# Kernel tuning notes

Measured on AMD Instinct MI355X. Metric: run time of the kernel, lower is better.

## Reference

```python
import jax, jax.numpy as jnp
import numpy as np

B = 8192
D_IN = 1024
D_H = 1024


def _lin(x, w, b):
    # torch nn.Linear: y = x @ w.T + b, w: [out, in]
    return x @ w.T + b


def setup_inputs() -> dict:
    key = jax.random.key(0)
    ks = iter(jax.random.split(key, 64))
    s = 0.02

    def w(shape):
        return (jax.random.normal(next(ks), shape, dtype=jnp.float32) * s)

    inp = {
        "x": jax.random.normal(next(ks), (B, D_IN), dtype=jnp.float32),
        "h_prev": jax.random.normal(next(ks), (B, D_H), dtype=jnp.float32),
        "c_prev": jax.random.normal(next(ks), (B, D_H), dtype=jnp.float32),
    }
    for name in ["Wi", "Wf", "Wo", "Wc", "Ws"]:
        inp[name + "_w"] = w((D_H, D_IN))
        inp[name + "_b"] = w((D_H,))
    for name in ["Ui", "Uf", "Uo", "Uc", "Us"]:
        inp[name + "_w"] = w((D_H, D_H))
        inp[name + "_b"] = w((D_H,))
    # alpha_mlp: Linear(in+h -> h), ReLU, Linear(h -> 1), Sigmoid
    inp["a1_w"] = w((D_H, D_IN + D_H)); inp["a1_b"] = w((D_H,))
    inp["a2_w"] = w((1, D_H)); inp["a2_b"] = w((1,))
    inp["r1_w"] = w((D_H, D_H)); inp["r1_b"] = w((D_H,))
    inp["r2_w"] = w((D_H, D_H)); inp["r2_b"] = w((D_H,))
    inp["r3_w"] = w((D_H, D_H)); inp["r3_b"] = w((D_H,))
    return inp


def reference(x, h_prev, c_prev,
              Wi_w, Wi_b, Wf_w, Wf_b, Wo_w, Wo_b, Wc_w, Wc_b, Ws_w, Ws_b,
              Ui_w, Ui_b, Uf_w, Uf_b, Uo_w, Uo_b, Uc_w, Uc_b, Us_w, Us_b,
              a1_w, a1_b, a2_w, a2_b,
              r1_w, r1_b, r2_w, r2_b, r3_w, r3_b):
    i_t = jax.nn.sigmoid(_lin(x, Wi_w, Wi_b) + _lin(h_prev, Ui_w, Ui_b))
    f_t = jax.nn.sigmoid(_lin(x, Wf_w, Wf_b) + _lin(h_prev, Uf_w, Uf_b))
    o_t = jax.nn.sigmoid(_lin(x, Wo_w, Wo_b) + _lin(h_prev, Uo_w, Uo_b))
    c_hat_t = jnp.tanh(_lin(x, Wc_w, Wc_b) + _lin(h_prev, Uc_w, Uc_b))

    combined = jnp.concatenate([x, h_prev], axis=-1)  # [B, D_IN + D_H]
    alpha_t = jax.nn.sigmoid(_lin(jax.nn.relu(_lin(combined, a1_w, a1_b)), a2_w, a2_b))  # [B, 1]

    s_t = jax.nn.sigmoid(_lin(x, Ws_w, Ws_b) + _lin(h_prev, Us_w, Us_b))

    c_t = f_t * c_prev + i_t * c_hat_t * s_t * alpha_t

    residual = _lin(jax.nn.relu(_lin(jax.nn.relu(_lin(h_prev, r1_w, r1_b)), r2_w, r2_b)), r3_w, r3_b)
    c_t = c_t + residual
    h_t = o_t * jnp.tanh(c_t)
    return (h_t, c_t)
```

## Files before the change

### kernel.cpp

```cpp
#include <hip/hip_runtime.h>
#include <hip/hip_bf16.h>

typedef __bf16 bf16;
typedef __bf16 bf16x8 __attribute__((ext_vector_type(8)));
typedef __bf16 bf16x4 __attribute__((ext_vector_type(4)));
typedef float f32x4 __attribute__((ext_vector_type(4)));

#define NBIG 7168
#define KBIG 2048

__device__ __forceinline__ float sigmoid_f(float x) { return 1.0f / (1.0f + __expf(-x)); }
__device__ __forceinline__ float tanh_f(float x) { return 1.0f - 2.0f / (__expf(2.0f * x) + 1.0f); }

__device__ __forceinline__ void gload_lds16(const bf16* g, bf16* lds) {
  __builtin_amdgcn_global_load_lds(
      (const __attribute__((address_space(1))) unsigned int*)g,
      (__attribute__((address_space(3))) unsigned int*)lds,
      16, 0, 0);
}


__global__ __launch_bounds__(256) void build_A(const float* __restrict__ x,
                                               const float* __restrict__ h,
                                               bf16* __restrict__ A) {
  const int i4 = blockIdx.x * 256 + threadIdx.x;
  const int o = i4 * 4;
  const int m = o >> 11;
  const int c = o & 2047;
  const float4 v = (c < 1024) ? *(const float4*)&x[(size_t)m * 1024 + c]
                              : *(const float4*)&h[(size_t)m * 1024 + (c - 1024)];
  bf16x4 b;
  b[0] = (bf16)v.x; b[1] = (bf16)v.y; b[2] = (bf16)v.z; b[3] = (bf16)v.w;
  *(bf16x4*)&A[(size_t)o] = b;
}

__global__ __launch_bounds__(256) void build_WG(
    const float* __restrict__ Wi, const float* __restrict__ Wf, const float* __restrict__ Wo,
    const float* __restrict__ Wc, const float* __restrict__ Ws,
    const float* __restrict__ Ui, const float* __restrict__ Uf, const float* __restrict__ Uo,
    const float* __restrict__ Uc, const float* __restrict__ Us,
    const float* __restrict__ a1w, const float* __restrict__ r1w, bf16* __restrict__ WG) {
  const int i4 = blockIdx.x * 256 + threadIdx.x;
  const int o = i4 * 4;
  const int n = o >> 11;
  const int c = o & 2047;
  const int g = n >> 10;
  const int r = n & 1023;
  float4 v;
  if (g < 5) {
    const float* Wp = g == 0 ? Wi : g == 1 ? Wf : g == 2 ? Wo : g == 3 ? Wc : Ws;
    const float* Up = g == 0 ? Ui : g == 1 ? Uf : g == 2 ? Uo : g == 3 ? Uc : Us;
    v = (c < 1024) ? *(const float4*)&Wp[(size_t)r * 1024 + c]
                   : *(const float4*)&Up[(size_t)r * 1024 + (c - 1024)];
  } else if (g == 5) {
    v = *(const float4*)&a1w[(size_t)r * 2048 + c];
  } else {
    if (c < 1024) { v.x = 0.f; v.y = 0.f; v.z = 0.f; v.w = 0.f; }
    else v = *(const float4*)&r1w[(size_t)r * 1024 + (c - 1024)];
  }
  bf16x4 b;
  b[0] = (bf16)v.x; b[1] = (bf16)v.y; b[2] = (bf16)v.z; b[3] = (bf16)v.w;
  *(bf16x4*)&WG[(size_t)o] = b;
}

__global__ __launch_bounds__(256) void build_bias(
    const float* __restrict__ Wib, const float* __restrict__ Wfb, const float* __restrict__ Wob,
    const float* __restrict__ Wcb, const float* __restrict__ Wsb,
    const float* __restrict__ Uib, const float* __restrict__ Ufb, const float* __restrict__ Uob,
    const float* __restrict__ Ucb, const float* __restrict__ Usb,
    const float* __restrict__ a1b, const float* __restrict__ r1b, float* __restrict__ bias) {
  const int n = blockIdx.x * 256 + threadIdx.x;
  if (n >= NBIG) return;
  const int g = n >> 10, r = n & 1023;
  float v;
  if (g < 5) {
    const float* Wb = g == 0 ? Wib : g == 1 ? Wfb : g == 2 ? Wob : g == 3 ? Wcb : Wsb;
    const float* Ub = g == 0 ? Uib : g == 1 ? Ufb : g == 2 ? Uob : g == 3 ? Ucb : Usb;
    v = Wb[r] + Ub[r];
  } else if (g == 5) v = a1b[r];
  else v = r1b[r];
  bias[n] = v;
}

__global__ __launch_bounds__(256) void f2b(const float* __restrict__ s, bf16* __restrict__ d,
                                           int n4) {
  const int i = blockIdx.x * 256 + threadIdx.x;
  if (i >= n4) return;
  const float4 v = *(const float4*)&s[(size_t)i * 4];
  bf16x4 b;
  b[0] = (bf16)v.x; b[1] = (bf16)v.y; b[2] = (bf16)v.z; b[3] = (bf16)v.w;
  *(bf16x4*)&d[(size_t)i * 4] = b;
}


#define BAR __builtin_amdgcn_s_barrier()
#define VM4 asm volatile("s_waitcnt vmcnt(4)" ::: "memory")
#define VM0 asm volatile("s_waitcnt vmcnt(0)" ::: "memory")
#define PRIO1 __builtin_amdgcn_s_setprio(1)
#define PRIO0 __builtin_amdgcn_s_setprio(0)

__global__ __launch_bounds__(256, 3) void gemm128(
    const bf16* __restrict__ A, int lda,
    const bf16* __restrict__ W, int ldw, int K,
    const float* __restrict__ bias,
    bf16* __restrict__ C, int ldc, int act_mode, int mtiles) {
  __shared__ __align__(16) bf16 sA[3][128 * 32];
  __shared__ __align__(16) bf16 sB[3][128 * 32];

  const int tid = threadIdx.x;
  const int lane = tid & 63;
  const int wv = tid >> 6;
  const int wr = wv >> 1, wc = wv & 1;

  int bmi, bni;
  if (gridDim.x == 3584) {
    const int xcd = blockIdx.x & 7;
    const int idx = blockIdx.x >> 3;
    bmi = (xcd >> 1) * 16 + idx / 28;
    bni = (xcd & 1) * 28 + idx % 28;
  } else {
    bmi = blockIdx.x % mtiles;
    bni = blockIdx.x / mtiles;
  }
  const int bm = bmi * 128;
  const int bn = bni * 128;

  const int srow = tid >> 2;
  const int scol = ((tid & 3) ^ ((tid >> 3) & 3)) * 8;
  const bf16* pA = A + (size_t)(bm + srow) * lda + scol;
  const bf16* pB = W + (size_t)(bn + srow) * ldw + scol;

  const int fr = lane & 15;
  const int lg = lane >> 4;
  const int sw16 = (lg ^ ((fr >> 1) & 3)) << 4;

  const int NT = K >> 5;

  f32x4 acc[4][4] = {};
  bf16x8 ar[4], br[4];

#define STGT(bb, tt)                                                \
  do {                                                              \
    const bf16* gA = pA + (size_t)(tt) * 32;                        \
    bf16* lA = &sA[bb][(wv * 16) * 32];                             \
    gload_lds16(gA, lA);                                            \
    gload_lds16(gA + (size_t)64 * lda, lA + 64 * 32);               \
    const bf16* gB = pB + (size_t)(tt) * 32;                        \
    bf16* lB = &sB[bb][(wv * 16) * 32];                             \
    gload_lds16(gB, lB);                                            \
    gload_lds16(gB + (size_t)64 * ldw, lB + 64 * 32);               \
  } while (0)
#define LDF(bb)                                                                  \
  do {                                                                           \
    _Pragma("unroll") for (int mi = 0; mi < 4; ++mi)                             \
        ar[mi] = *(const bf16x8*)((const char*)&sA[bb][0] +                      \
            (wr * 64 + mi * 16 + fr) * 64 + sw16);                               \
    _Pragma("unroll") for (int nj = 0; nj < 4; ++nj)                             \
        br[nj] = *(const bf16x8*)((const char*)&sB[bb][0] +                      \
            (wc * 64 + nj * 16 + fr) * 64 + sw16);                               \
  } while (0)
#define MM()                                                                     \
  do {                                                                           \
    _Pragma("unroll") for (int mi = 0; mi < 4; ++mi)                             \
    _Pragma("unroll") for (int nj = 0; nj < 4; ++nj)                             \
      acc[mi][nj] = __builtin_amdgcn_mfma_f32_16x16x32_bf16(                     \
          ar[mi], br[nj], acc[mi][nj], 0, 0, 0);                                 \
  } while (0)

  STGT(0, 0);
  STGT(1, 1);
  VM4; BAR;

  int bld = 0;
  int bst = 2;
  for (int t = 0; t + 2 < NT; ++t) {
    STGT(bst, t + 2);
    LDF(bld);
    PRIO1; MM(); PRIO0;
    VM4;
    BAR;
    bld = bld == 2 ? 0 : bld + 1;
    bst = bst == 2 ? 0 : bst + 1;
  }

  LDF(bld);
  PRIO1; MM(); PRIO0;
  VM0; BAR;
  bld = bld == 2 ? 0 : bld + 1;
  LDF(bld);
  PRIO1; MM(); PRIO0;

  const int rbase = lg * 4;
#pragma unroll
  for (int j = 0; j < 4; ++j) {
    const int n = bn + wc * 64 + j * 16 + fr;
    const float bv = bias[n];
    const int g = (act_mode == 0) ? (n >> 10) : (act_mode == 1 ? 100 : 101);
#pragma unroll
    for (int mi = 0; mi < 4; ++mi) {
      const size_t mrow = (size_t)(bm + wr * 64 + mi * 16 + rbase);
#pragma unroll
      for (int r = 0; r < 4; ++r) {
        float v = acc[mi][j][r] + bv;
        if (g == 3) v = tanh_f(v);
        else if (g < 5) v = sigmoid_f(v);
        else if (g < 7 || g == 100) v = fmaxf(v, 0.0f);
        C[(mrow + r) * (size_t)ldc + n] = (bf16)v;
      }
    }
  }
#undef STGT
#undef LDF
#undef MM
}

__global__ __launch_bounds__(256) void alpha_k(const bf16* __restrict__ G,
                                               const float* __restrict__ a2w,
                                               const float* __restrict__ a2b,
                                               float* __restrict__ alpha) {
  const int m = blockIdx.x * 4 + (threadIdx.x >> 6);
  const int lane = threadIdx.x & 63;
  const bf16* row = G + (size_t)m * NBIG + 5120 + lane * 16;
  const bf16x8 v0 = *(const bf16x8*)row;
  const bf16x8 v1 = *(const bf16x8*)(row + 8);
  const float* w = a2w + lane * 16;
  float s = 0.f;
#pragma unroll
  for (int e = 0; e < 8; ++e) s += (float)v0[e] * w[e] + (float)v1[e] * w[8 + e];
#pragma unroll
  for (int off = 32; off > 0; off >>= 1) s += __shfl_down(s, off, 64);
  if (lane == 0) alpha[m] = sigmoid_f(s + a2b[0]);
}

__global__ __launch_bounds__(256) void final_k(const bf16* __restrict__ G,
                                               const bf16* __restrict__ R3,
                                               const float* __restrict__ c_prev,
                                               const float* __restrict__ alpha,
                                               float* __restrict__ out) {
  const int idx = blockIdx.x * 256 + threadIdx.x;
  const int o = idx * 8;
  const int m = o >> 10;
  const int c = o & 1023;
  const size_t gb = (size_t)m * NBIG;
  const bf16x8 iv = *(const bf16x8*)&G[gb + c];
  const bf16x8 fv = *(const bf16x8*)&G[gb + 1024 + c];
  const bf16x8 ov = *(const bf16x8*)&G[gb + 2048 + c];
  const bf16x8 cv = *(const bf16x8*)&G[gb + 3072 + c];
  const bf16x8 sv = *(const bf16x8*)&G[gb + 4096 + c];
  const bf16x8 rv = *(const bf16x8*)&R3[(size_t)m * 1024 + c];
  const float al = alpha[m];
  const float* cp = &c_prev[(size_t)m * 1024 + c];
  float hbuf[8], cbuf[8];
#pragma unroll
  for (int e = 0; e < 8; ++e) {
    const float ct = (float)fv[e] * cp[e] + (float)iv[e] * (float)cv[e] * (float)sv[e] * al
                     + (float)rv[e];
    cbuf[e] = ct;
    hbuf[e] = (float)ov[e] * tanh_f(ct);
  }
  float* oh = out + (size_t)m * 1024 + c;
  float* oc = out + (size_t)8192 * 1024 + (size_t)m * 1024 + c;
#pragma unroll
  for (int e = 0; e < 8; ++e) { oh[e] = hbuf[e]; oc[e] = cbuf[e]; }
}

extern "C" void kernel_launch(void* const* d_in, const int* in_sizes, int n_in,
                              void* d_out, int out_size, void* d_ws, size_t ws_size,
                              hipStream_t stream) {
  const float* x      = (const float*)d_in[0];
  const float* h_prev = (const float*)d_in[1];
  const float* c_prev = (const float*)d_in[2];
  const float* Wi_w = (const float*)d_in[3];  const float* Wi_b = (const float*)d_in[4];
  const float* Wf_w = (const float*)d_in[5];  const float* Wf_b = (const float*)d_in[6];
  const float* Wo_w = (const float*)d_in[7];  const float* Wo_b = (const float*)d_in[8];
  const float* Wc_w = (const float*)d_in[9];  const float* Wc_b = (const float*)d_in[10];
  const float* Ws_w = (const float*)d_in[11]; const float* Ws_b = (const float*)d_in[12];
  const float* Ui_w = (const float*)d_in[13]; const float* Ui_b = (const float*)d_in[14];
  const float* Uf_w = (const float*)d_in[15]; const float* Uf_b = (const float*)d_in[16];
  const float* Uo_w = (const float*)d_in[17]; const float* Uo_b = (const float*)d_in[18];
  const float* Uc_w = (const float*)d_in[19]; const float* Uc_b = (const float*)d_in[20];
  const float* Us_w = (const float*)d_in[21]; const float* Us_b = (const float*)d_in[22];
  const float* a1_w = (const float*)d_in[23]; const float* a1_b = (const float*)d_in[24];
  const float* a2_w = (const float*)d_in[25]; const float* a2_b = (const float*)d_in[26];
  const float* r1_w = (const float*)d_in[27]; const float* r1_b = (const float*)d_in[28];
  const float* r2_w = (const float*)d_in[29]; const float* r2_b = (const float*)d_in[30];
  const float* r3_w = (const float*)d_in[31]; const float* r3_b = (const float*)d_in[32];

  char* ws = (char*)d_ws;
  size_t off = 0;
  auto alloc = [&](size_t bytes) -> void* {
    void* p = ws + off;
    off += (bytes + 255) & ~(size_t)255;
    return p;
  };
  bf16* A_big    = (bf16*)alloc((size_t)8192 * 2048 * 2);
  bf16* WG       = (bf16*)alloc((size_t)7168 * 2048 * 2);
  float* bias_bg = (float*)alloc((size_t)7168 * 4);
  bf16* WR2      = (bf16*)alloc((size_t)1024 * 1024 * 2);
  bf16* WR3      = (bf16*)alloc((size_t)1024 * 1024 * 2);
  bf16* G        = (bf16*)alloc((size_t)8192 * 7168 * 2);
  bf16* R2       = (bf16*)alloc((size_t)8192 * 1024 * 2);
  bf16* R3       = (bf16*)alloc((size_t)8192 * 1024 * 2);
  float* alpha   = (float*)alloc((size_t)8192 * 4);

  build_A<<<16384, 256, 0, stream>>>(x, h_prev, A_big);
  build_WG<<<14336, 256, 0, stream>>>(Wi_w, Wf_w, Wo_w, Wc_w, Ws_w,
                                      Ui_w, Uf_w, Uo_w, Uc_w, Us_w, a1_w, r1_w, WG);
  build_bias<<<28, 256, 0, stream>>>(Wi_b, Wf_b, Wo_b, Wc_b, Ws_b,
                                     Ui_b, Uf_b, Uo_b, Uc_b, Us_b, a1_b, r1_b, bias_bg);
  f2b<<<1024, 256, 0, stream>>>(r2_w, WR2, 262144);
  f2b<<<1024, 256, 0, stream>>>(r3_w, WR3, 262144);

  gemm128<<<3584, 256, 0, stream>>>(A_big, 2048, WG, 2048, 2048, bias_bg, G, NBIG, 0, 64);

  alpha_k<<<2048, 256, 0, stream>>>(G, a2_w, a2_b, alpha);

  gemm128<<<512, 256, 0, stream>>>(G + 6144, NBIG, WR2, 1024, 1024, r2_b, R2, 1024, 1, 64);
  gemm128<<<512, 256, 0, stream>>>(R2, 1024, WR3, 1024, 1024, r3_b, R3, 1024, 2, 64);

  final_k<<<4096, 256, 0, stream>>>(G, R3, c_prev, alpha, (float*)d_out);
}
```

Before: 446.5 us.

## Use 256x256 tile GEMM for fused gate projection and skip zero K-half

Replaces the 128x128 tile GEMM for the big fused gate/alpha/residual projection with a 1024-thread 256x256 tile kernel using BK=64, double-buffered LDS and an XCD-aware tile mapping. For the residual r1 columns, whose weights are zero over the x half of K, it starts the K loop at the midpoint to skip the zero work. build_WG no longer writes those zero weights, and the two r2/r3 weight conversions are merged into one launch. The larger tile raises operand reuse but uses 128KB of LDS and two barriers per step, which limits occupancy and may hurt latency hiding.

```diff
diff --git a/kernel.cpp b/kernel.cpp
--- a/kernel.cpp
+++ b/kernel.cpp
@@ -55,8 +55,8 @@
   } else if (g == 5) {
     v = *(const float4*)&a1w[(size_t)r * 2048 + c];
   } else {
-    if (c < 1024) { v.x = 0.f; v.y = 0.f; v.z = 0.f; v.w = 0.f; }
-    else v = *(const float4*)&r1w[(size_t)r * 1024 + (c - 1024)];
+    if (c < 1024) return;
+    v = *(const float4*)&r1w[(size_t)r * 1024 + (c - 1024)];
   }
   bf16x4 b;
   b[0] = (bf16)v.x; b[1] = (bf16)v.y; b[2] = (bf16)v.z; b[3] = (bf16)v.w;
@@ -82,14 +82,18 @@
   bias[n] = v;
 }
 
-__global__ __launch_bounds__(256) void f2b(const float* __restrict__ s, bf16* __restrict__ d,
-                                           int n4) {
+__global__ __launch_bounds__(256) void f2b2(const float* __restrict__ s0,
+                                            const float* __restrict__ s1,
+                                            bf16* __restrict__ d0, bf16* __restrict__ d1) {
   const int i = blockIdx.x * 256 + threadIdx.x;
-  if (i >= n4) return;
-  const float4 v = *(const float4*)&s[(size_t)i * 4];
+  const int which = i >> 18;
+  const int j = i & 262143;
+  const float* s = which ? s1 : s0;
+  bf16* d = which ? d1 : d0;
+  const float4 v = *(const float4*)&s[(size_t)j * 4];
   bf16x4 b;
   b[0] = (bf16)v.x; b[1] = (bf16)v.y; b[2] = (bf16)v.z; b[3] = (bf16)v.w;
-  *(bf16x4*)&d[(size_t)i * 4] = b;
+  *(bf16x4*)&d[(size_t)j * 4] = b;
 }
 
 
@@ -98,6 +102,124 @@
 #define VM0 asm volatile("s_waitcnt vmcnt(0)" ::: "memory")
 #define PRIO1 __builtin_amdgcn_s_setprio(1)
 #define PRIO0 __builtin_amdgcn_s_setprio(0)
+
+__global__ __launch_bounds__(1024, 4) void gemm256(
+    const bf16* __restrict__ A, int lda,
+    const bf16* __restrict__ W, int ldw, int K,
+    const float* __restrict__ bias,
+    bf16* __restrict__ C, int ldc, int act_mode, int mtiles) {
+  __shared__ __align__(16) bf16 sA[2][256 * 64];
+  __shared__ __align__(16) bf16 sB[2][256 * 64];
+
+  const int tid = threadIdx.x;
+  const int lane = tid & 63;
+  const int wv = tid >> 6;
+  const int wr = wv >> 2;
+  const int wc = wv & 3;
+
+  int bmi, bni;
+  if (gridDim.x == 896) {
+    const int xcd = blockIdx.x & 7;
+    const int idx = blockIdx.x >> 3;
+    bmi = (xcd >> 2) * 16 + idx / 7;
+    bni = (xcd & 3) * 7 + idx % 7;
+  } else {
+    bmi = blockIdx.x % mtiles;
+    bni = blockIdx.x / mtiles;
+  }
+  const int bm = bmi * 256;
+  const int bn = bni * 256;
+
+  const int kt0 = (act_mode == 0 && bni >= 24) ? 16 : 0;
+
+  const int srow = tid >> 3;
+  const int scol = ((tid & 7) ^ (srow & 7)) * 8;
+  const bf16* pA = A + (size_t)(bm + srow) * lda + scol + (size_t)kt0 * 64;
+  const bf16* pB = W + (size_t)(bn + srow) * ldw + scol + (size_t)kt0 * 64;
+
+  const int fr = lane & 15;
+  const int lg = lane >> 4;
+  const int off0 = (lg * 16) ^ ((fr & 7) << 4);
+
+  const int NT = (K >> 6) - kt0;
+
+  f32x4 acc[4][4] = {};
+  bf16x8 ar[4], br[4];
+
+#define STGT(bb, tt)                                                        \
+  do {                                                                      \
+    const bf16* gA = pA + (size_t)(tt) * 64;                                \
+    gload_lds16(gA, &sA[bb][(wv * 8) * 64]);                                \
+    gload_lds16(gA + (size_t)128 * lda, &sA[bb][(128 + wv * 8) * 64]);      \
+    const bf16* gB = pB + (size_t)(tt) * 64;                                \
+    gload_lds16(gB, &sB[bb][(wv * 8) * 64]);                                \
+    gload_lds16(gB + (size_t)128 * ldw, &sB[bb][(128 + wv * 8) * 64]);      \
+  } while (0)
+#define LDF(bb, kkc)                                                             \
+  do {                                                                           \
+    _Pragma("unroll") for (int mi = 0; mi < 4; ++mi)                             \
+        ar[mi] = *(const bf16x8*)((const char*)&sA[bb][0] +                      \
+            (wr * 64 + mi * 16 + fr) * 128 + (off0 ^ ((kkc) << 6)));             \
+    _Pragma("unroll") for (int nj = 0; nj < 4; ++nj)                             \
+        br[nj] = *(const bf16x8*)((const char*)&sB[bb][0] +                      \
+            (wc * 64 + nj * 16 + fr) * 128 + (off0 ^ ((kkc) << 6)));             \
+  } while (0)
+#define MM()                                                                     \
+  do {                                                                           \
+    _Pragma("unroll") for (int mi = 0; mi < 4; ++mi)                             \
+    _Pragma("unroll") for (int nj = 0; nj < 4; ++nj)                             \
+      acc[mi][nj] = __builtin_amdgcn_mfma_f32_16x16x32_bf16(                     \
+          ar[mi], br[nj], acc[mi][nj], 0, 0, 0);                                 \
+  } while (0)
+
+  STGT(0, 0);
+  STGT(1, 1);
+  VM4; BAR;
+
+  for (int t = 0; t + 2 < NT; ++t) {
+    const int b = t & 1;
+    LDF(b, 0);
+    PRIO1; MM(); PRIO0;
+    LDF(b, 1);
+    PRIO1; MM(); PRIO0;
+    BAR;
+    STGT(b, t + 2);
+    VM4;
+    BAR;
+  }
+
+  {
+    const int b = NT & 1;
+    LDF(b, 0); PRIO1; MM(); PRIO0;
+    LDF(b, 1); PRIO1; MM(); PRIO0;
+    BAR; VM0; BAR;
+    LDF(b ^ 1, 0); PRIO1; MM(); PRIO0;
+    LDF(b ^ 1, 1); PRIO1; MM(); PRIO0;
+  }
+
+  const int rbase = lg * 4;
+#pragma unroll
+  for (int j = 0; j < 4; ++j) {
+    const int n = bn + wc * 64 + j * 16 + fr;
+    const float bv = bias[n];
+    const int g = (act_mode == 0) ? (n >> 10) : (act_mode == 1 ? 100 : 101);
+#pragma unroll
+    for (int mi = 0; mi < 4; ++mi) {
+      const size_t mrow = (size_t)(bm + wr * 64 + mi * 16 + rbase);
+#pragma unroll
+      for (int r = 0; r < 4; ++r) {
+        float v = acc[mi][j][r] + bv;
+        if (g == 3) v = tanh_f(v);
+        else if (g < 5) v = sigmoid_f(v);
+        else if (g < 7 || g == 100) v = fmaxf(v, 0.0f);
+        C[(mrow + r) * (size_t)ldc + n] = (bf16)v;
+      }
+    }
+  }
+#undef STGT
+#undef LDF
+#undef MM
+}
 
 __global__ __launch_bounds__(256, 3) void gemm128(
     const bf16* __restrict__ A, int lda,
@@ -112,16 +234,8 @@
   const int wv = tid >> 6;
   const int wr = wv >> 1, wc = wv & 1;
 
-  int bmi, bni;
-  if (gridDim.x == 3584) {
-    const int xcd = blockIdx.x & 7;
-    const int idx = blockIdx.x >> 3;
-    bmi = (xcd >> 1) * 16 + idx / 28;
-    bni = (xcd & 1) * 28 + idx % 28;
-  } else {
-    bmi = blockIdx.x % mtiles;
-    bni = blockIdx.x / mtiles;
-  }
+  const int bmi = blockIdx.x % mtiles;
+  const int bni = blockIdx.x / mtiles;
   const int bm = bmi * 128;
   const int bn = bni * 128;
 
@@ -171,8 +285,7 @@
   STGT(1, 1);
   VM4; BAR;
 
-  int bld = 0;
-  int bst = 2;
+  int bld = 0, bst = 2;
   for (int t = 0; t + 2 < NT; ++t) {
     STGT(bst, t + 2);
     LDF(bld);
@@ -308,10 +421,9 @@
                                       Ui_w, Uf_w, Uo_w, Uc_w, Us_w, a1_w, r1_w, WG);
   build_bias<<<28, 256, 0, stream>>>(Wi_b, Wf_b, Wo_b, Wc_b, Ws_b,
                                      Ui_b, Uf_b, Uo_b, Uc_b, Us_b, a1_b, r1_b, bias_bg);
-  f2b<<<1024, 256, 0, stream>>>(r2_w, WR2, 262144);
-  f2b<<<1024, 256, 0, stream>>>(r3_w, WR3, 262144);
-
-  gemm128<<<3584, 256, 0, stream>>>(A_big, 2048, WG, 2048, 2048, bias_bg, G, NBIG, 0, 64);
+  f2b2<<<2048, 256, 0, stream>>>(r2_w, r3_w, WR2, WR3);
+
+  gemm256<<<896, 1024, 0, stream>>>(A_big, 2048, WG, 2048, 2048, bias_bg, G, NBIG, 0, 32);
 
   alpha_k<<<2048, 256, 0, stream>>>(G, a2_w, a2_b, alpha);
 
```

Result: faster. 399.9 us (median of 2 runs) (-10.4%).
